# Optimization experiments

Hardware: AMD Instinct MI355X
Metric: run time of the kernel (lower is better)

Reference implementation:

```python
import jax, jax.numpy as jnp
import numpy as np

LPOS, LDIR, H = 10, 4, 256
N = 262144


def posenc(x, L):
    freqs = (2.0 ** jnp.arange(L)).astype(x.dtype)  # [L]
    ang = x[:, None, :] * freqs[:, None]            # [N, L, 3]
    sc = jnp.concatenate([jnp.sin(ang), jnp.cos(ang)], axis=-1)  # [N, L, 6]
    return jnp.concatenate([x, sc.reshape(x.shape[0], L * 6)], axis=1)


def _lin(key, fan_in, fan_out):
    k1, k2 = jax.random.split(key)
    bound = 1.0 / np.sqrt(fan_in)
    w = jax.random.uniform(k1, (fan_out, fan_in), jnp.float32, -bound, bound)
    b = jax.random.uniform(k2, (fan_out,), jnp.float32, -bound, bound)
    return w, b


def setup_inputs() -> dict:
    key = jax.random.key(0)
    ks = jax.random.split(key, 16)
    inp = {
        'xyz': jax.random.normal(ks[0], (N, 3), jnp.float32),
        'd': jax.random.normal(ks[1], (N, 3), jnp.float32),
    }
    in1 = LPOS * 6 + 3  # 63
    dims1 = [(in1, H), (H, H), (H, H), (H, H), (H, H)]
    for i, (fi, fo) in enumerate(dims1):
        w, b = _lin(ks[2 + i], fi, fo)
        inp[f'w1_{i}'], inp[f'b1_{i}'] = w, b
    dims2 = [(H + in1, H), (H, H), (H, H), (H, H + 1)]
    for i, (fi, fo) in enumerate(dims2):
        w, b = _lin(ks[7 + i], fi, fo)
        inp[f'w2_{i}'], inp[f'b2_{i}'] = w, b
    w, b = _lin(ks[11], H + LDIR * 6 + 3, H // 2)
    inp['wr0'], inp['br0'] = w, b
    w, b = _lin(ks[12], H // 2, 3)
    inp['wr1'], inp['br1'] = w, b
    return inp


def reference(xyz, d,
              w1_0, b1_0, w1_1, b1_1, w1_2, b1_2, w1_3, b1_3, w1_4, b1_4,
              w2_0, b2_0, w2_1, b2_1, w2_2, b2_2, w2_3, b2_3,
              wr0, br0, wr1, br1):
    relu = jax.nn.relu
    x_emb = posenc(xyz, LPOS)  # [N, 63]
    d_emb = posenc(d, LDIR)    # [N, 27]
    h = x_emb
    for w, b in ((w1_0, b1_0), (w1_1, b1_1), (w1_2, b1_2), (w1_3, b1_3), (w1_4, b1_4)):
        h = relu(h @ w.T + b)
    h = jnp.concatenate([h, x_emb], axis=1)
    for w, b in ((w2_0, b2_0), (w2_1, b2_1), (w2_2, b2_2)):
        h = relu(h @ w.T + b)
    h = h @ w2_3.T + b2_3  # [N, H+1]
    sigma = h[:, -1]
    h = h[:, :-1]
    # rgb head
    g = relu(jnp.concatenate([h, d_emb], axis=1) @ wr0.T + br0)
    c = jax.nn.sigmoid(g @ wr1.T + br1)  # [N, 3]
    return c, relu(sigma)
```

## Files before the change

kernel.cpp:

```cpp
#include <hip/hip_runtime.h>
#include <hip/hip_bf16.h>

#define NPTS 262144
#define ROWS 64
#define SA 328
#define SB 264
#define LDS_BYTES ((ROWS*SA + ROWS*SB)*2)

typedef __attribute__((ext_vector_type(8))) short short8;
typedef __attribute__((ext_vector_type(4))) float f32x4;

__device__ __forceinline__ ushort bfu(float f) {
  union { float f; unsigned u; } x; x.f = f;
  unsigned r = x.u + 0x7fffu + ((x.u >> 16) & 1u);
  return (ushort)(r >> 16);
}

__device__ __forceinline__ unsigned pk2(float a, float b) {
  __hip_bfloat162 h = __float22bfloat162_rn(float2{a, b});
  return *reinterpret_cast<unsigned*>(&h);
}

__global__ void pack_w(const float* __restrict__ w, ushort* __restrict__ dst,
                       int OUT, int KIN, int nct, int nkt) {
  int t = blockIdx.x * 256 + threadIdx.x;
  int total = nct * nkt * 64;
  if (t >= total) return;
  int l  = t & 63;
  int kt = (t >> 6) % nkt;
  int ct = (t >> 6) / nkt;
  int row = ct * 16 + (l & 15);
  int k0  = kt * 32 + (l >> 4) * 8;
  ushort* d = dst + (size_t)t * 8;
  #pragma unroll
  for (int j = 0; j < 8; ++j) {
    int k = k0 + j;
    float v = (row < OUT && k < KIN) ? w[(size_t)row * KIN + k] : 0.f;
    d[j] = bfu(v);
  }
}

__global__ void pack_b(const float* __restrict__ b, float* __restrict__ dst, int OUT, int OUTP) {
  int i = blockIdx.x * 256 + threadIdx.x;
  if (i < OUTP) dst[i] = (i < OUT) ? b[i] : 0.f;
}

template<int NKT, int KSPLIT, int NC, bool RELU>
__device__ __forceinline__ void layerg(
    const ushort* __restrict__ wpk, const float* __restrict__ bias,
    const ushort* a0, int s0, const ushort* a1, int s1,
    ushort* dst, int sd, int dstCol0,
    int ctBase, int lane)
{
  const int lr = lane & 15, lk = lane >> 4;
  f32x4 acc[4][NC];
  #pragma unroll
  for (int c = 0; c < NC; ++c) {
    f32x4 b4 = *(const f32x4*)(bias + (ctBase + c) * 16 + lk * 4);
    #pragma unroll
    for (int r = 0; r < 4; ++r) acc[r][c] = b4;
  }
  #pragma unroll 4
  for (int kt = 0; kt < NKT; ++kt) {
    short8 av[4];
    if (kt < KSPLIT) {
      int ko = kt * 32 + lk * 8;
      #pragma unroll
      for (int r = 0; r < 4; ++r)
        av[r] = *(const short8*)(a0 + (size_t)(r * 16 + lr) * s0 + ko);
    } else {
      int ko = (kt - KSPLIT) * 32 + lk * 8;
      #pragma unroll
      for (int r = 0; r < 4; ++r)
        av[r] = *(const short8*)(a1 + (size_t)(r * 16 + lr) * s1 + ko);
    }
    #pragma unroll
    for (int c = 0; c < NC; ++c) {
      short8 bv = *(const short8*)(wpk + (size_t)(((ctBase + c) * NKT + kt) * 64 + lane) * 8);
      #pragma unroll
      for (int r = 0; r < 4; ++r)
        acc[r][c] = __builtin_amdgcn_mfma_f32_16x16x32_bf16(bv, av[r], acc[r][c], 0, 0, 0);
    }
  }
  #pragma unroll
  for (int c = 0; c < NC; ++c)
    #pragma unroll
    for (int r = 0; r < 4; ++r) {
      float v0 = acc[r][c][0], v1 = acc[r][c][1], v2 = acc[r][c][2], v3 = acc[r][c][3];
      if (RELU) {
        v0 = fmaxf(v0, 0.f); v1 = fmaxf(v1, 0.f);
        v2 = fmaxf(v2, 0.f); v3 = fmaxf(v3, 0.f);
      }
      uint2 p; p.x = pk2(v0, v1); p.y = pk2(v2, v3);
      *(uint2*)(dst + (size_t)(r * 16 + lr) * sd + dstCol0 + (ctBase + c) * 16 + lk * 4) = p;
    }
}

extern __shared__ ushort smem[];

__global__ __launch_bounds__(512, 4) void nerf_fused(
    const float* __restrict__ xyz, const float* __restrict__ dvec,
    const ushort* __restrict__ wp, const float* __restrict__ bp,
    float* __restrict__ out)
{
  ushort* bufA = smem;
  ushort* bufB = smem + ROWS * SA;
  const int tid  = threadIdx.x;
  const int row0 = blockIdx.x * ROWS;
  const int wave = tid >> 6, lane = tid & 63;
  const int lr = lane & 15, lk = lane >> 4;

  {
    int r = tid >> 3, j = tid & 7;
    const float* x = xyz + (size_t)(row0 + r) * 3;
    float x0 = x[0], x1 = x[1], x2 = x[2];
    ushort* dst = bufA + (size_t)r * SA + 256;
    if (j == 7) { dst[0] = bfu(x0); dst[1] = bfu(x1); dst[2] = bfu(x2); dst[63] = 0; }
    for (int l = j; l < 10; l += 8) {
      float f = (float)(1 << l);
      int b = 3 + l * 6;
      dst[b + 0] = bfu(__sinf(x0 * f)); dst[b + 1] = bfu(__sinf(x1 * f)); dst[b + 2] = bfu(__sinf(x2 * f));
      dst[b + 3] = bfu(__cosf(x0 * f)); dst[b + 4] = bfu(__cosf(x1 * f)); dst[b + 5] = bfu(__cosf(x2 * f));
    }
  }
  __syncthreads();
  layerg<2, 2, 2, true >(wp + 0,      bp + 0,    bufA + 256, SA, bufA, SA, bufB, SB, 0, wave * 2, lane);
  __syncthreads();
  layerg<8, 8, 2, true >(wp + 16384,  bp + 256,  bufB, SB, bufB, SB, bufA, SA, 0, wave * 2, lane);
  __syncthreads();
  layerg<8, 8, 2, true >(wp + 81920,  bp + 512,  bufA, SA, bufA, SA, bufB, SB, 0, wave * 2, lane);
  __syncthreads();
  layerg<8, 8, 2, true >(wp + 147456, bp + 768,  bufB, SB, bufB, SB, bufA, SA, 0, wave * 2, lane);
  __syncthreads();
  layerg<8, 8, 2, true >(wp + 212992, bp + 1024, bufA, SA, bufA, SA, bufB, SB, 0, wave * 2, lane);
  __syncthreads();
  layerg<10, 8, 2, true>(wp + 278528, bp + 1280, bufB, SB, bufA + 256, SA, bufA, SA, 0, wave * 2, lane);
  __syncthreads();
  layerg<8, 8, 2, true >(wp + 360448, bp + 1536, bufA, SA, bufA, SA, bufB, SB, 0, wave * 2, lane);
  __syncthreads();
  layerg<8, 8, 2, true >(wp + 425984, bp + 1792, bufB, SB, bufB, SB, bufA, SA, 0, wave * 2, lane);
  __syncthreads();
  layerg<8, 8, 2, false>(wp + 491520, bp + 2048, bufA, SA, bufA, SA, bufB, SB, 0, wave * 2, lane);
  if (wave == 0) {
    const ushort* w23 = wp + 491520;
    float bb = bp[2048 + 256 + lr];
    f32x4 acc2[4];
    #pragma unroll
    for (int r = 0; r < 4; ++r) acc2[r] = (f32x4){bb, bb, bb, bb};
    #pragma unroll 2
    for (int kt = 0; kt < 8; ++kt) {
      short8 bv = *(const short8*)(w23 + (size_t)((16 * 8 + kt) * 64 + lane) * 8);
      #pragma unroll
      for (int r = 0; r < 4; ++r) {
        short8 av = *(const short8*)(bufA + (size_t)(r * 16 + lr) * SA + kt * 32 + lk * 8);
        acc2[r] = __builtin_amdgcn_mfma_f32_16x16x32_bf16(av, bv, acc2[r], 0, 0, 0);
      }
    }
    if (lr == 0) {
      #pragma unroll
      for (int r = 0; r < 4; ++r)
        #pragma unroll
        for (int i = 0; i < 4; ++i)
          out[(size_t)3 * NPTS + row0 + r * 16 + lk * 4 + i] = fmaxf(acc2[r][i], 0.f);
    }
  }
  __syncthreads();
  {
    int r = tid >> 3, j = tid & 7;
    const float* x = dvec + (size_t)(row0 + r) * 3;
    float x0 = x[0], x1 = x[1], x2 = x[2];
    ushort* dst = bufA + (size_t)r * SA;
    if (j == 7) {
      dst[0] = bfu(x0); dst[1] = bfu(x1); dst[2] = bfu(x2);
      #pragma unroll
      for (int q = 27; q < 32; ++q) dst[q] = 0;
    }
    if (j < 4) {
      float f = (float)(1 << j);
      int b = 3 + j * 6;
      dst[b + 0] = bfu(__sinf(x0 * f)); dst[b + 1] = bfu(__sinf(x1 * f)); dst[b + 2] = bfu(__sinf(x2 * f));
      dst[b + 3] = bfu(__cosf(x0 * f)); dst[b + 4] = bfu(__cosf(x1 * f)); dst[b + 5] = bfu(__cosf(x2 * f));
    }
  }
  __syncthreads();
  layerg<9, 8, 1, true>(wp + 561152, bp + 2320, bufB, SB, bufA, SA, bufA, SA, 128, wave, lane);
  __syncthreads();
  if (wave < 4) {
    const ushort* w = wp + 598016;
    float bb = bp[2448 + lr];
    f32x4 acc = (f32x4){bb, bb, bb, bb};
    #pragma unroll
    for (int kt = 0; kt < 4; ++kt) {
      short8 av = *(const short8*)(bufA + (size_t)(wave * 16 + lr) * SA + 128 + kt * 32 + lk * 8);
      short8 bv = *(const short8*)(w + (size_t)(kt * 64 + lane) * 8);
      acc = __builtin_amdgcn_mfma_f32_16x16x32_bf16(av, bv, acc, 0, 0, 0);
    }
    if (lr < 3) {
      #pragma unroll
      for (int i = 0; i < 4; ++i) {
        int grow = row0 + wave * 16 + lk * 4 + i;
        out[(size_t)grow * 3 + lr] = 1.f / (1.f + __expf(-acc[i]));
      }
    }
  }
}

extern "C" void kernel_launch(void* const* d_in, const int* in_sizes, int n_in,
                              void* d_out, int out_size, void* d_ws, size_t ws_size,
                              hipStream_t stream) {
  const float* xyz  = (const float*)d_in[0];
  const float* dvec = (const float*)d_in[1];
  ushort* wp = (ushort*)d_ws;
  float*  bp = (float*)((char*)d_ws + 1200128);

  struct WSpec { int idx, OUT, KIN, nct, nkt, off; };
  const WSpec wspecs[11] = {
    { 2, 256,  63, 16,  2,      0},
    { 4, 256, 256, 16,  8,  16384},
    { 6, 256, 256, 16,  8,  81920},
    { 8, 256, 256, 16,  8, 147456},
    {10, 256, 256, 16,  8, 212992},
    {12, 256, 319, 16, 10, 278528},
    {14, 256, 256, 16,  8, 360448},
    {16, 256, 256, 16,  8, 425984},
    {18, 257, 256, 17,  8, 491520},
    {20, 128, 283,  8,  9, 561152},
    {22,   3, 128,  1,  4, 598016},
  };
  for (int i = 0; i < 11; ++i) {
    int total = wspecs[i].nct * wspecs[i].nkt * 64;
    pack_w<<<dim3((total + 255) / 256), dim3(256), 0, stream>>>(
      (const float*)d_in[wspecs[i].idx], wp + wspecs[i].off,
      wspecs[i].OUT, wspecs[i].KIN, wspecs[i].nct, wspecs[i].nkt);
  }
  struct BSpec { int idx, OUT, OUTP, off; };
  const BSpec bspecs[11] = {
    { 3, 256, 256,    0}, { 5, 256, 256,  256}, { 7, 256, 256,  512}, { 9, 256, 256,  768},
    {11, 256, 256, 1024}, {13, 256, 256, 1280}, {15, 256, 256, 1536}, {17, 256, 256, 1792},
    {19, 257, 272, 2048}, {21, 128, 128, 2320}, {23,   3,  16, 2448},
  };
  for (int i = 0; i < 11; ++i) {
    pack_b<<<dim3((bspecs[i].OUTP + 255) / 256), dim3(256), 0, stream>>>(
      (const float*)d_in[bspecs[i].idx], bp + bspecs[i].off, bspecs[i].OUT, bspecs[i].OUTP);
  }

  hipFuncSetAttribute(reinterpret_cast<const void*>(nerf_fused),
                      hipFuncAttributeMaxDynamicSharedMemorySize, LDS_BYTES);
  nerf_fused<<<dim3(NPTS / ROWS), dim3(512), LDS_BYTES, stream>>>(xyz, dvec, wp, bp, (float*)d_out);
}
```

Baseline: 370.3 us.

## Store activations in MFMA fragment layout and overlap direction encoding with layers

Activation buffers in LDS now use a fragment-major layout: each 16-row by 32-column tile is a contiguous 512-element block indexed by lane. A-operand loads become conflict-free contiguous 16-byte reads instead of strided row reads, and the epilogue writes outputs directly in that layout. Positional encodings go into a separate small xbuf, built per fragment with vectorized stores. The direction encoding is computed by four waves during the block-2 layers, which removes one barrier. K loops are now fully unrolled, which raises register pressure.

```diff
diff --git a/kernel.cpp b/kernel.cpp
--- a/kernel.cpp
+++ b/kernel.cpp
@@ -3,9 +3,10 @@
 
 #define NPTS 262144
 #define ROWS 64
-#define SA 328
-#define SB 264
-#define LDS_BYTES ((ROWS*SA + ROWS*SB)*2)
+#define FR 512
+#define BUF1_OFF 16384
+#define XBUF_OFF 32768
+#define LDS_BYTES ((16384*2 + 4096)*2)
 
 typedef __attribute__((ext_vector_type(8))) short short8;
 typedef __attribute__((ext_vector_type(4))) float f32x4;
@@ -15,7 +16,6 @@
   unsigned r = x.u + 0x7fffu + ((x.u >> 16) & 1u);
   return (ushort)(r >> 16);
 }
-
 __device__ __forceinline__ unsigned pk2(float a, float b) {
   __hip_bfloat162 h = __float22bfloat162_rn(float2{a, b});
   return *reinterpret_cast<unsigned*>(&h);
@@ -48,9 +48,8 @@
 template<int NKT, int KSPLIT, int NC, bool RELU>
 __device__ __forceinline__ void layerg(
     const ushort* __restrict__ wpk, const float* __restrict__ bias,
-    const ushort* a0, int s0, const ushort* a1, int s1,
-    ushort* dst, int sd, int dstCol0,
-    int ctBase, int lane)
+    const ushort* a0, const ushort* a1, int rs1,
+    ushort* dst, int ctBase, int lane)
 {
   const int lr = lane & 15, lk = lane >> 4;
   f32x4 acc[4][NC];
@@ -60,19 +59,15 @@
     #pragma unroll
     for (int r = 0; r < 4; ++r) acc[r][c] = b4;
   }
-  #pragma unroll 4
+  #pragma unroll
   for (int kt = 0; kt < NKT; ++kt) {
     short8 av[4];
-    if (kt < KSPLIT) {
-      int ko = kt * 32 + lk * 8;
-      #pragma unroll
-      for (int r = 0; r < 4; ++r)
-        av[r] = *(const short8*)(a0 + (size_t)(r * 16 + lr) * s0 + ko);
-    } else {
-      int ko = (kt - KSPLIT) * 32 + lk * 8;
-      #pragma unroll
-      for (int r = 0; r < 4; ++r)
-        av[r] = *(const short8*)(a1 + (size_t)(r * 16 + lr) * s1 + ko);
+    #pragma unroll
+    for (int r = 0; r < 4; ++r) {
+      const ushort* src = (kt < KSPLIT)
+        ? (a0 + (r * 8 + kt) * FR + lane * 8)
+        : (a1 + (r * rs1 + (kt - KSPLIT)) * FR + lane * 8);
+      av[r] = *(const short8*)src;
     }
     #pragma unroll
     for (int c = 0; c < NC; ++c) {
@@ -83,7 +78,10 @@
     }
   }
   #pragma unroll
-  for (int c = 0; c < NC; ++c)
+  for (int c = 0; c < NC; ++c) {
+    const int ct = ctBase + c;
+    const int Lp = lr + 16 * ((ct & 1) * 2 + (lk >> 1));
+    const int kq = ct >> 1;
     #pragma unroll
     for (int r = 0; r < 4; ++r) {
       float v0 = acc[r][c][0], v1 = acc[r][c][1], v2 = acc[r][c][2], v3 = acc[r][c][3];
@@ -92,8 +90,9 @@
         v2 = fmaxf(v2, 0.f); v3 = fmaxf(v3, 0.f);
       }
       uint2 p; p.x = pk2(v0, v1); p.y = pk2(v2, v3);
-      *(uint2*)(dst + (size_t)(r * 16 + lr) * sd + dstCol0 + (ctBase + c) * 16 + lk * 4) = p;
-    }
+      *(uint2*)(dst + (r * 8 + kq) * FR + Lp * 8 + (lk & 1) * 4) = p;
+    }
+  }
 }
 
 extern __shared__ ushort smem[];
@@ -103,56 +102,98 @@
     const ushort* __restrict__ wp, const float* __restrict__ bp,
     float* __restrict__ out)
 {
-  ushort* bufA = smem;
-  ushort* bufB = smem + ROWS * SA;
+  ushort* buf0 = smem;
+  ushort* buf1 = smem + BUF1_OFF;
+  ushort* xbuf = smem + XBUF_OFF;
   const int tid  = threadIdx.x;
   const int row0 = blockIdx.x * ROWS;
   const int wave = tid >> 6, lane = tid & 63;
   const int lr = lane & 15, lk = lane >> 4;
 
   {
-    int r = tid >> 3, j = tid & 7;
-    const float* x = xyz + (size_t)(row0 + r) * 3;
-    float x0 = x[0], x1 = x[1], x2 = x[2];
-    ushort* dst = bufA + (size_t)r * SA + 256;
-    if (j == 7) { dst[0] = bfu(x0); dst[1] = bfu(x1); dst[2] = bfu(x2); dst[63] = 0; }
-    for (int l = j; l < 10; l += 8) {
-      float f = (float)(1 << l);
-      int b = 3 + l * 6;
-      dst[b + 0] = bfu(__sinf(x0 * f)); dst[b + 1] = bfu(__sinf(x1 * f)); dst[b + 2] = bfu(__sinf(x2 * f));
-      dst[b + 3] = bfu(__cosf(x0 * f)); dst[b + 4] = bfu(__cosf(x1 * f)); dst[b + 5] = bfu(__cosf(x2 * f));
-    }
-  }
-  __syncthreads();
-  layerg<2, 2, 2, true >(wp + 0,      bp + 0,    bufA + 256, SA, bufA, SA, bufB, SB, 0, wave * 2, lane);
-  __syncthreads();
-  layerg<8, 8, 2, true >(wp + 16384,  bp + 256,  bufB, SB, bufB, SB, bufA, SA, 0, wave * 2, lane);
-  __syncthreads();
-  layerg<8, 8, 2, true >(wp + 81920,  bp + 512,  bufA, SA, bufA, SA, bufB, SB, 0, wave * 2, lane);
-  __syncthreads();
-  layerg<8, 8, 2, true >(wp + 147456, bp + 768,  bufB, SB, bufB, SB, bufA, SA, 0, wave * 2, lane);
-  __syncthreads();
-  layerg<8, 8, 2, true >(wp + 212992, bp + 1024, bufA, SA, bufA, SA, bufB, SB, 0, wave * 2, lane);
-  __syncthreads();
-  layerg<10, 8, 2, true>(wp + 278528, bp + 1280, bufB, SB, bufA + 256, SA, bufA, SA, 0, wave * 2, lane);
-  __syncthreads();
-  layerg<8, 8, 2, true >(wp + 360448, bp + 1536, bufA, SA, bufA, SA, bufB, SB, 0, wave * 2, lane);
-  __syncthreads();
-  layerg<8, 8, 2, true >(wp + 425984, bp + 1792, bufB, SB, bufB, SB, bufA, SA, 0, wave * 2, lane);
-  __syncthreads();
-  layerg<8, 8, 2, false>(wp + 491520, bp + 2048, bufA, SA, bufA, SA, bufB, SB, 0, wave * 2, lane);
+    const int r = wave & 3, kt = wave >> 2;
+    const float* x = xyz + (size_t)(row0 + r * 16 + lr) * 3;
+    float xv[3] = {x[0], x[1], x[2]};
+    const int c0 = kt * 32 + lk * 8;
+    unsigned u[4];
+    #pragma unroll
+    for (int q = 0; q < 4; ++q) {
+      ushort h2[2];
+      #pragma unroll
+      for (int hh = 0; hh < 2; ++hh) {
+        int c = c0 + q * 2 + hh;
+        float v;
+        if (c < 3) v = xv[c];
+        else if (c < 63) {
+          int idx = c - 3, l = idx / 6, t = idx - l * 6;
+          float f = (float)(1 << l);
+          float xx = xv[t < 3 ? t : t - 3];
+          v = (t < 3) ? __sinf(xx * f) : __cosf(xx * f);
+        } else v = 0.f;
+        h2[hh] = bfu(v);
+      }
+      u[q] = (unsigned)h2[0] | ((unsigned)h2[1] << 16);
+    }
+    uint4* dstv = (uint4*)(xbuf + (r * 2 + kt) * FR + lane * 8);
+    *dstv = make_uint4(u[0], u[1], u[2], u[3]);
+  }
+  __syncthreads();
+  layerg<2, 0, 2, true >(wp + 0,      bp + 0,    buf0, xbuf, 2, buf0, wave * 2, lane);
+  __syncthreads();
+  layerg<8, 8, 2, true >(wp + 16384,  bp + 256,  buf0, xbuf, 2, buf1, wave * 2, lane);
+  __syncthreads();
+  layerg<8, 8, 2, true >(wp + 81920,  bp + 512,  buf1, xbuf, 2, buf0, wave * 2, lane);
+  __syncthreads();
+  layerg<8, 8, 2, true >(wp + 147456, bp + 768,  buf0, xbuf, 2, buf1, wave * 2, lane);
+  __syncthreads();
+  layerg<8, 8, 2, true >(wp + 212992, bp + 1024, buf1, xbuf, 2, buf0, wave * 2, lane);
+  __syncthreads();
+  layerg<10, 8, 2, true>(wp + 278528, bp + 1280, buf0, xbuf, 2, buf1, wave * 2, lane);
+  __syncthreads();
+  if (wave < 4) {
+    const int r = wave;
+    const float* d = dvec + (size_t)(row0 + r * 16 + lr) * 3;
+    float dv[3] = {d[0], d[1], d[2]};
+    const int c0 = lk * 8;
+    unsigned u[4];
+    #pragma unroll
+    for (int q = 0; q < 4; ++q) {
+      ushort h2[2];
+      #pragma unroll
+      for (int hh = 0; hh < 2; ++hh) {
+        int c = c0 + q * 2 + hh;
+        float v;
+        if (c < 3) v = dv[c];
+        else if (c < 27) {
+          int idx = c - 3, l = idx / 6, t = idx - l * 6;
+          float f = (float)(1 << l);
+          float xx = dv[t < 3 ? t : t - 3];
+          v = (t < 3) ? __sinf(xx * f) : __cosf(xx * f);
+        } else v = 0.f;
+        h2[hh] = bfu(v);
+      }
+      u[q] = (unsigned)h2[0] | ((unsigned)h2[1] << 16);
+    }
+    uint4* dstv = (uint4*)(xbuf + r * FR + lane * 8);
+    *dstv = make_uint4(u[0], u[1], u[2], u[3]);
+  }
+  layerg<8, 8, 2, true >(wp + 360448, bp + 1536, buf1, xbuf, 2, buf0, wave * 2, lane);
+  __syncthreads();
+  layerg<8, 8, 2, true >(wp + 425984, bp + 1792, buf0, xbuf, 2, buf1, wave * 2, lane);
+  __syncthreads();
+  layerg<8, 8, 2, false>(wp + 491520, bp + 2048, buf1, xbuf, 2, buf0, wave * 2, lane);
   if (wave == 0) {
     const ushort* w23 = wp + 491520;
     float bb = bp[2048 + 256 + lr];
     f32x4 acc2[4];
     #pragma unroll
     for (int r = 0; r < 4; ++r) acc2[r] = (f32x4){bb, bb, bb, bb};
-    #pragma unroll 2
+    #pragma unroll
     for (int kt = 0; kt < 8; ++kt) {
       short8 bv = *(const short8*)(w23 + (size_t)((16 * 8 + kt) * 64 + lane) * 8);
       #pragma unroll
       for (int r = 0; r < 4; ++r) {
-        short8 av = *(const short8*)(bufA + (size_t)(r * 16 + lr) * SA + kt * 32 + lk * 8);
+        short8 av = *(const short8*)(buf1 + (r * 8 + kt) * FR + lane * 8);
         acc2[r] = __builtin_amdgcn_mfma_f32_16x16x32_bf16(av, bv, acc2[r], 0, 0, 0);
       }
     }
@@ -165,25 +206,7 @@
     }
   }
   __syncthreads();
-  {
-    int r = tid >> 3, j = tid & 7;
-    const float* x = dvec + (size_t)(row0 + r) * 3;
-    float x0 = x[0], x1 = x[1], x2 = x[2];
-    ushort* dst = bufA + (size_t)r * SA;
-    if (j == 7) {
-      dst[0] = bfu(x0); dst[1] = bfu(x1); dst[2] = bfu(x2);
-      #pragma unroll
-      for (int q = 27; q < 32; ++q) dst[q] = 0;
-    }
-    if (j < 4) {
-      float f = (float)(1 << j);
-      int b = 3 + j * 6;
-      dst[b + 0] = bfu(__sinf(x0 * f)); dst[b + 1] = bfu(__sinf(x1 * f)); dst[b + 2] = bfu(__sinf(x2 * f));
-      dst[b + 3] = bfu(__cosf(x0 * f)); dst[b + 4] = bfu(__cosf(x1 * f)); dst[b + 5] = bfu(__cosf(x2 * f));
-    }
-  }
-  __syncthreads();
-  layerg<9, 8, 1, true>(wp + 561152, bp + 2320, bufB, SB, bufA, SA, bufA, SA, 128, wave, lane);
+  layerg<9, 8, 1, true>(wp + 561152, bp + 2320, buf0, xbuf, 1, buf1, wave, lane);
   __syncthreads();
   if (wave < 4) {
     const ushort* w = wp + 598016;
@@ -191,7 +214,7 @@
     f32x4 acc = (f32x4){bb, bb, bb, bb};
     #pragma unroll
     for (int kt = 0; kt < 4; ++kt) {
-      short8 av = *(const short8*)(bufA + (size_t)(wave * 16 + lr) * SA + 128 + kt * 32 + lk * 8);
+      short8 av = *(const short8*)(buf1 + (wave * 8 + kt) * FR + lane * 8);
       short8 bv = *(const short8*)(w + (size_t)(kt * 64 + lane) * 8);
       acc = __builtin_amdgcn_mfma_f32_16x16x32_bf16(av, bv, acc, 0, 0, 0);
     }
```

Measured after the change: 338.1 us. -8.7%, faster.
